# Optimization experiments

Hardware: AMD Instinct MI355X
Metric: run time of the kernel (lower is better)

## Reference

```python
import jax, jax.numpy as jnp
import numpy as np

B, N, K = 8, 2048, 16   # batch, points, neighbors (after dropping self)
EPS = 1e-5


def _bn(y, g, b, m, v):
    # eval-mode batchnorm over channel dim 1, y: [B,C,...]
    sh = (1, -1) + (1,) * (y.ndim - 2)
    inv = g.reshape(sh) / jnp.sqrt(v.reshape(sh) + EPS)
    return (y - m.reshape(sh)) * inv + b.reshape(sh)


def setup_inputs() -> dict:
    key = jax.random.key(0)
    ks = jax.random.split(key, 16)
    d = {}
    d["x"] = jax.random.normal(ks[0], (B, 3, N), dtype=jnp.float32)
    # pre: Conv1d(3->24, k=1) + BN
    d["w_pre"] = jax.random.normal(ks[1], (24, 3), dtype=jnp.float32) * 0.3
    d["b_pre"] = jax.random.normal(ks[2], (24,), dtype=jnp.float32) * 0.1
    d["g_pre"] = 1.0 + 0.1 * jax.random.normal(ks[3], (24,), dtype=jnp.float32)
    d["be_pre"] = 0.1 * jax.random.normal(ks[4], (24,), dtype=jnp.float32)
    d["m_pre"] = 0.1 * jax.random.normal(ks[5], (24,), dtype=jnp.float32)
    d["v_pre"] = jax.random.uniform(ks[6], (24,), minval=0.5, maxval=1.5, dtype=jnp.float32)
    # shared_mlp_1: Conv2d(48->12, 1, bias=False) + BN
    d["w1"] = jax.random.normal(ks[7], (12, 48), dtype=jnp.float32) * 0.15
    d["g1"] = 1.0 + 0.1 * jax.random.normal(ks[8], (12,), dtype=jnp.float32)
    d["be1"] = 0.1 * jax.random.normal(ks[9], (12,), dtype=jnp.float32)
    d["m1"] = 0.1 * jax.random.normal(ks[10], (12,), dtype=jnp.float32)
    d["v1"] = jax.random.uniform(ks[11], (12,), minval=0.5, maxval=1.5, dtype=jnp.float32)
    # shared_mlp_2: Conv2d(60->12, 1, bias=False) + BN
    d["w2"] = jax.random.normal(ks[12], (12, 60), dtype=jnp.float32) * 0.15
    d["g2"] = 1.0 + 0.1 * jax.random.normal(ks[13], (12,), dtype=jnp.float32)
    d["be2"] = 0.1 * jax.random.normal(ks[14], (12,), dtype=jnp.float32)
    d["m2"] = 0.1 * jax.random.normal(ks[15], (12,), dtype=jnp.float32)
    d["v2"] = jnp.ones((12,), dtype=jnp.float32)
    # shared_mlp_3: Conv2d(72->12, 1, bias=False), no BN
    d["w3"] = jax.random.normal(jax.random.fold_in(key, 99), (12, 72), dtype=jnp.float32) * 0.15
    return d


def reference(x, w_pre, b_pre, g_pre, be_pre, m_pre, v_pre,
              w1, g1, be1, m1, v1, w2, g2, be2, m2, v2, w3):
    # pre: 1x1 conv1d + BN + ReLU -> [B,24,N]
    pre = jnp.einsum('oc,bcn->bon', w_pre, x) + b_pre[None, :, None]
    pre = jax.nn.relu(_bn(pre, g_pre, be_pre, m_pre, v_pre))

    # kNN on xyz = x.detach(): [B,N,3]
    pts = jax.lax.stop_gradient(jnp.swapaxes(x, 1, 2))
    sq = jnp.sum(pts * pts, axis=-1)                              # [B,N]
    d2 = sq[:, :, None] + sq[:, None, :] - 2.0 * jnp.einsum('bnc,bmc->bnm', pts, pts)
    _, idx = jax.lax.top_k(-d2, K + 1)                             # nearest K+1 incl. self
    idx = idx[..., 1:]                                             # drop self -> [B,N,K]

    # gather neighbor features: [B,24,N,K]
    grouped = jax.vmap(lambda f, i: f[:, i])(pre, idx)
    center = jnp.broadcast_to(pre[..., None], grouped.shape)
    y = jnp.concatenate([center, grouped], axis=1)                 # [B,48,N,K]

    h1 = jax.nn.relu(_bn(jnp.einsum('oc,bcnk->bonk', w1, y), g1, be1, m1, v1))
    y = jnp.concatenate([h1, y], axis=1)                           # [B,60,N,K]
    h2 = jax.nn.relu(_bn(jnp.einsum('oc,bcnk->bonk', w2, y), g2, be2, m2, v2))
    y = jnp.concatenate([h2, y], axis=1)                           # [B,72,N,K]
    h3 = jnp.einsum('oc,bcnk->bonk', w3, y)
    y = jnp.concatenate([h3, y], axis=1)                           # [B,84,N,K]

    y = jnp.max(y, axis=-1)                                        # maxpool over neighbors -> [B,84,N]
    return jnp.concatenate([y, x], axis=1)                         # [B,87,N]
```

## Files before the change

kernel.cpp:

```cpp
#include <hip/hip_runtime.h>
#include <math.h>

#define EPS 1e-5f
#define NBATCH 8
#define NPTS 2048
#define KNB 16
#define BIG 3.2e38f

#define PRE_BLKS 32
#define KNN_BLKS (NBATCH * 64)
#define FUSED_LDS 54400

#define WS_PRE 0
#define WS_AUX (16384 * 24)
#define WS_IDX (WS_AUX + 16384 * 72)

__global__ __launch_bounds__(512) void fused_kernel(
    const float* __restrict__ x,
    const float* __restrict__ w_pre, const float* __restrict__ b_pre,
    const float* __restrict__ g_pre, const float* __restrict__ be_pre,
    const float* __restrict__ m_pre, const float* __restrict__ v_pre,
    const float* __restrict__ w1, const float* __restrict__ g1,
    const float* __restrict__ be1, const float* __restrict__ m1,
    const float* __restrict__ v1,
    const float* __restrict__ w2, const float* __restrict__ g2,
    const float* __restrict__ be2, const float* __restrict__ m2,
    const float* __restrict__ v2, const float* __restrict__ w3,
    float* __restrict__ pre, float* __restrict__ aux,
    int* __restrict__ knn_out) {
  extern __shared__ char smem[];
  int tid = threadIdx.x;
  if (blockIdx.x < PRE_BLKS) {
    float* fwp = (float*)smem;
    float* fbp = fwp + 72;
    float* fw1 = fbp + 24;
    float* fb1 = fw1 + 576;
    float* fw2 = fb1 + 12;
    float* fb2 = fw2 + 720;
    if (tid < 72) { int o = tid / 3; fwp[tid] = w_pre[tid] * (g_pre[o] / sqrtf(v_pre[o] + EPS)); }
    if (tid < 24) { float inv = g_pre[tid] / sqrtf(v_pre[tid] + EPS);
                    fbp[tid] = (b_pre[tid] - m_pre[tid]) * inv + be_pre[tid]; }
    for (int j = tid; j < 576; j += 512) { int o = j / 48; fw1[j] = w1[j] * (g1[o] / sqrtf(v1[o] + EPS)); }
    if (tid < 12) { float inv = g1[tid] / sqrtf(v1[tid] + EPS); fb1[tid] = be1[tid] - m1[tid] * inv; }
    for (int j = tid; j < 720; j += 512) { int o = j / 60; fw2[j] = w2[j] * (g2[o] / sqrtf(v2[o] + EPS)); }
    if (tid < 12) { float inv = g2[tid] / sqrtf(v2[tid] + EPS); fb2[tid] = be2[tid] - m2[tid] * inv; }
    __syncthreads();
    int p = blockIdx.x * 512 + tid;
    int b = p >> 11, n = p & (NPTS - 1);
    const float* xb = x + (size_t)b * 3 * NPTS;
    float x0 = xb[n], x1 = xb[NPTS + n], x2 = xb[2 * NPTS + n];
    float pr[24];
#pragma unroll
    for (int c = 0; c < 24; ++c) {
      float v = fmaf(fwp[c * 3 + 0], x0,
                fmaf(fwp[c * 3 + 1], x1,
                fmaf(fwp[c * 3 + 2], x2, fbp[c])));
      pr[c] = fmaxf(v, 0.f);
    }
    float4* o4 = (float4*)(pre + (size_t)p * 24);
#pragma unroll
    for (int i = 0; i < 6; ++i)
      o4[i] = make_float4(pr[4*i], pr[4*i+1], pr[4*i+2], pr[4*i+3]);
    float* A = aux + (size_t)p * 72;
#pragma unroll
    for (int o = 0; o < 12; ++o) {
      float u1 = fb1[o], a1 = 0.f, u2 = fb2[o], a2 = 0.f, u3 = 0.f, a3 = 0.f;
#pragma unroll
      for (int i = 0; i < 24; ++i) {
        u1 = fmaf(fw1[o*48 + i],      pr[i], u1);
        a1 = fmaf(fw1[o*48 + 24 + i], pr[i], a1);
        u2 = fmaf(fw2[o*60 + 12 + i], pr[i], u2);
        a2 = fmaf(fw2[o*60 + 36 + i], pr[i], a2);
        u3 = fmaf(w3[o*72 + 24 + i],  pr[i], u3);
        a3 = fmaf(w3[o*72 + 48 + i],  pr[i], a3);
      }
      A[o] = u1; A[12+o] = u2; A[24+o] = u3;
      A[36+o] = a1; A[48+o] = a2; A[60+o] = a3;
    }
    return;
  }
  float4* C4   = (float4*)smem;
  float* slist = (float*)(smem + 32768);
  float* sd2   = (float*)(smem + 49152);
  int*   sidx  = (int*)(smem + 51712);
  int*   scnt  = (int*)(smem + 54272);
  int bi = blockIdx.x - PRE_BLKS;
  int b = bi >> 6, chunk = bi & 63;
  const float* xb = x + (size_t)b * 3 * NPTS;
  for (int j = tid; j < NPTS; j += 512) {
    float xx = xb[j], yy = xb[NPTS + j], zz = xb[2 * NPTS + j];
    float sq = __fadd_rn(__fadd_rn(__fmul_rn(xx, xx), __fmul_rn(yy, yy)),
                         __fmul_rn(zz, zz));
    C4[j] = make_float4(2.0f * xx, 2.0f * yy, 2.0f * zz, sq);
  }
  for (int j = tid; j < 32 * 20; j += 512) sidx[j] = 0;
  if (tid < 32) scnt[tid] = 0;
  __syncthreads();
  int p = tid & 31, s = tid >> 5;
  int n = chunk * 32 + p;
  float4 me4 = C4[n];
  float mex = 0.5f * me4.x, mey = 0.5f * me4.y, mez = 0.5f * me4.z;
  float sqn = me4.w;
  const float4* Cs = C4 + s * 128;
  int selfc = n - s * 128;
  float L[16];
#pragma unroll
  for (int t = 0; t < 16; ++t) L[t] = BIG;
#pragma unroll 4
  for (int c = 0; c < 128; ++c) {
    float4 q = Cs[c];
    float dot2 = __fadd_rn(__fadd_rn(__fmul_rn(mex, q.x), __fmul_rn(mey, q.y)),
                           __fmul_rn(mez, q.z));
    float d2 = __fsub_rn(__fadd_rn(sqn, q.w), dot2);
    d2 = (c == selfc) ? BIG : d2;
#pragma unroll
    for (int t = 15; t >= 1; --t) L[t] = fminf(fmaxf(L[t-1], d2), L[t]);
    L[0] = fminf(L[0], d2);
  }
  {
    float bb[16], m16[16];
#pragma unroll
    for (int i = 0; i < 16; ++i) bb[i] = __shfl_xor(L[i], 32, 64);
#pragma unroll
    for (int i = 0; i < 16; ++i) m16[i] = fminf(L[i], bb[15 - i]);
#pragma unroll
    for (int d = 8; d >= 1; d >>= 1) {
#pragma unroll
      for (int i = 0; i < 16; ++i) {
        if (!(i & d)) {
          float lo = fminf(m16[i], m16[i | d]);
          float hi = fmaxf(m16[i], m16[i | d]);
          m16[i] = lo; m16[i | d] = hi;
        }
      }
    }
    if (!(s & 1)) {
#pragma unroll
      for (int i = 0; i < 16; ++i) slist[((s >> 1) * 16 + i) * 32 + p] = m16[i];
    }
  }
  __syncthreads();
  for (int W = 4; W >= 1; W >>= 1) {
    int w = tid >> 5;
    bool act = (w < W);
    float a[16], bb[16];
    if (act) {
#pragma unroll
      for (int i = 0; i < 16; ++i) a[i]  = slist[((2 * w) * 16 + i) * 32 + p];
#pragma unroll
      for (int i = 0; i < 16; ++i) bb[i] = slist[((2 * w + 1) * 16 + i) * 32 + p];
    }
    __syncthreads();
    if (act) {
      float m16[16];
#pragma unroll
      for (int i = 0; i < 16; ++i) m16[i] = fminf(a[i], bb[15 - i]);
#pragma unroll
      for (int d = 8; d >= 1; d >>= 1) {
#pragma unroll
        for (int i = 0; i < 16; ++i) {
          if (!(i & d)) {
            float lo = fminf(m16[i], m16[i | d]);
            float hi = fmaxf(m16[i], m16[i | d]);
            m16[i] = lo; m16[i | d] = hi;
          }
        }
      }
#pragma unroll
      for (int i = 0; i < 16; ++i) slist[(w * 16 + i) * 32 + p] = m16[i];
    }
    __syncthreads();
  }
  float tau = slist[15 * 32 + p];
#pragma unroll 4
  for (int c = 0; c < 128; ++c) {
    float4 q = Cs[c];
    float dot2 = __fadd_rn(__fadd_rn(__fmul_rn(mex, q.x), __fmul_rn(mey, q.y)),
                           __fmul_rn(mez, q.z));
    float d2 = __fsub_rn(__fadd_rn(sqn, q.w), dot2);
    int j = s * 128 + c;
    if (d2 <= tau && j != n) {
      int pos = atomicAdd(&scnt[p], 1);
      if (pos < 20) { sd2[p * 20 + pos] = d2; sidx[p * 20 + pos] = j; }
    }
  }
  __syncthreads();
  if (tid < 32) {
    int c = scnt[tid]; if (c > 20) c = 20;
    if (c > 16) {
      for (int t = 0; t < 16; ++t) {
        int best = t;
        for (int u = t + 1; u < c; ++u) {
          float da = sd2[tid * 20 + u], db = sd2[tid * 20 + best];
          int ia = sidx[tid * 20 + u], ib = sidx[tid * 20 + best];
          if (da < db || (da == db && ia < ib)) best = u;
        }
        float td = sd2[tid * 20 + t]; sd2[tid * 20 + t] = sd2[tid * 20 + best]; sd2[tid * 20 + best] = td;
        int ti = sidx[tid * 20 + t]; sidx[tid * 20 + t] = sidx[tid * 20 + best]; sidx[tid * 20 + best] = ti;
      }
    }
  }
  __syncthreads();
  {
    int pp = tid >> 4, kk = tid & 15;
    knn_out[((size_t)b * NPTS + chunk * 32 + pp) * KNB + kk] = sidx[pp * 20 + kk];
  }
}

__global__ __launch_bounds__(256) void mlp_kernel(
    const float* __restrict__ pre, const float* __restrict__ aux,
    const int* __restrict__ knn, const float* __restrict__ x,
    const float* __restrict__ w2, const float* __restrict__ g2,
    const float* __restrict__ v2, const float* __restrict__ w3,
    float* __restrict__ out) {
  __shared__ float sW2h[144], sW3h2[144], sW3h1[144];
  __shared__ float sout[87 * 16];
  int tid = threadIdx.x;
  if (tid < 144) {
    int o = tid / 12, i = tid - o * 12;
    float inv2 = g2[o] / sqrtf(v2[o] + EPS);
    sW2h[tid]  = w2[o * 60 + i] * inv2;
    sW3h2[tid] = w3[o * 72 + i];
    sW3h1[tid] = w3[o * 72 + 12 + i];
  }
  __syncthreads();
  int k = tid & 15, pl = tid >> 4;
  int p = blockIdx.x * 16 + pl;
  int b = p >> 11, n = p & (NPTS - 1);
  int nb = knn[(size_t)p * KNB + k];
  const float4* u4 = (const float4*)(aux + (size_t)p * 72);
  const float4* a4 = (const float4*)(aux + ((size_t)(b << 11) + nb) * 72 + 36);
  float uc[36], av[36];
#pragma unroll
  for (int i = 0; i < 9; ++i) {
    float4 t = u4[i];
    uc[4*i] = t.x; uc[4*i+1] = t.y; uc[4*i+2] = t.z; uc[4*i+3] = t.w;
    float4 t2 = a4[i];
    av[4*i] = t2.x; av[4*i+1] = t2.y; av[4*i+2] = t2.z; av[4*i+3] = t2.w;
  }
  float h1[12], h2[12], h3[12];
#pragma unroll
  for (int o = 0; o < 12; ++o) h1[o] = fmaxf(uc[o] + av[o], 0.f);
#pragma unroll
  for (int o = 0; o < 12; ++o) {
    float a = uc[12 + o] + av[12 + o];
#pragma unroll
    for (int i = 0; i < 12; ++i) a = fmaf(sW2h[o * 12 + i], h1[i], a);
    h2[o] = fmaxf(a, 0.f);
  }
#pragma unroll
  for (int o = 0; o < 12; ++o) {
    float a = uc[24 + o] + av[24 + o];
#pragma unroll
    for (int i = 0; i < 12; ++i) a = fmaf(sW3h2[o * 12 + i], h2[i], a);
#pragma unroll
    for (int i = 0; i < 12; ++i) a = fmaf(sW3h1[o * 12 + i], h1[i], a);
    h3[o] = a;
  }
  float nbf[24];
  const float4* pn4 = (const float4*)(pre + ((size_t)(b << 11) + nb) * 24);
#pragma unroll
  for (int i = 0; i < 6; ++i) {
    float4 t = pn4[i];
    nbf[4*i] = t.x; nbf[4*i+1] = t.y; nbf[4*i+2] = t.z; nbf[4*i+3] = t.w;
  }
#pragma unroll
  for (int m = 1; m < 16; m <<= 1) {
#pragma unroll
    for (int o = 0; o < 12; ++o) {
      h1[o] = fmaxf(h1[o], __shfl_xor(h1[o], m, 16));
      h2[o] = fmaxf(h2[o], __shfl_xor(h2[o], m, 16));
      h3[o] = fmaxf(h3[o], __shfl_xor(h3[o], m, 16));
    }
#pragma unroll
    for (int i = 0; i < 24; ++i)
      nbf[i] = fmaxf(nbf[i], __shfl_xor(nbf[i], m, 16));
  }
  if (k == 0) {
    const float4* c4 = (const float4*)(pre + (size_t)p * 24);
#pragma unroll
    for (int o = 0; o < 12; ++o) {
      sout[(0  + o) * 16 + pl] = h3[o];
      sout[(12 + o) * 16 + pl] = h2[o];
      sout[(24 + o) * 16 + pl] = h1[o];
    }
#pragma unroll
    for (int i = 0; i < 6; ++i) {
      float4 t = c4[i];
      sout[(36 + 4*i    ) * 16 + pl] = t.x;
      sout[(36 + 4*i + 1) * 16 + pl] = t.y;
      sout[(36 + 4*i + 2) * 16 + pl] = t.z;
      sout[(36 + 4*i + 3) * 16 + pl] = t.w;
    }
#pragma unroll
    for (int i = 0; i < 24; ++i) sout[(60 + i) * 16 + pl] = nbf[i];
    const float* xb = x + (size_t)b * 3 * NPTS + n;
    sout[84 * 16 + pl] = xb[0];
    sout[85 * 16 + pl] = xb[NPTS];
    sout[86 * 16 + pl] = xb[2 * NPTS];
  }
  __syncthreads();
  int n0 = (blockIdx.x * 16) & (NPTS - 1);
  float* ob = out + (size_t)b * 87 * NPTS;
  for (int j2 = tid; j2 < 87 * 16; j2 += 256) {
    int c = j2 >> 4, i = j2 & 15;
    ob[(size_t)c * NPTS + n0 + i] = sout[j2];
  }
}

extern "C" void kernel_launch(void* const* d_in, const int* in_sizes, int n_in,
                              void* d_out, int out_size, void* d_ws, size_t ws_size,
                              hipStream_t stream) {
  (void)in_sizes; (void)n_in; (void)out_size; (void)ws_size;
  const float* x     = (const float*)d_in[0];
  const float* w_pre = (const float*)d_in[1];
  const float* b_pre = (const float*)d_in[2];
  const float* g_pre = (const float*)d_in[3];
  const float* be_pre= (const float*)d_in[4];
  const float* m_pre = (const float*)d_in[5];
  const float* v_pre = (const float*)d_in[6];
  const float* w1    = (const float*)d_in[7];
  const float* g1    = (const float*)d_in[8];
  const float* be1   = (const float*)d_in[9];
  const float* m1    = (const float*)d_in[10];
  const float* v1    = (const float*)d_in[11];
  const float* w2    = (const float*)d_in[12];
  const float* g2    = (const float*)d_in[13];
  const float* be2   = (const float*)d_in[14];
  const float* m2    = (const float*)d_in[15];
  const float* v2    = (const float*)d_in[16];
  const float* w3    = (const float*)d_in[17];
  float* ws  = (float*)d_ws;
  float* pre = ws + WS_PRE;
  float* aux = ws + WS_AUX;
  int*   knn = (int*)(ws + WS_IDX);
  float* out = (float*)d_out;

  fused_kernel<<<PRE_BLKS + KNN_BLKS, 512, FUSED_LDS, stream>>>(
      x, w_pre, b_pre, g_pre, be_pre, m_pre, v_pre,
      w1, g1, be1, m1, v1, w2, g2, be2, m2, v2, w3,
      pre, aux, knn);
  mlp_kernel<<<NBATCH * NPTS / 16, 256, 0, stream>>>(pre, aux, knn, x,
                                                     w2, g2, v2, w3, out);
}
```

Before: 178.3 us.

## Fold pre-MLP into KNN blocks and batch top-K insertion with bitonic merges

Removes the separate pre-compute blocks: every KNN block now computes the pre features and aux partial products for its own 32 points, with 16 threads per point each handling one output channel. The per-candidate 16-deep insertion in the KNN scan is replaced by sorting chunks of 16 distances with a bitonic network and merging each chunk into the running list. The distance uses FMA instead of separately rounded multiplies and adds, and launch bounds request 4 blocks per CU. The FMA change can alter rounding, and with it the neighbor choice in near-tie cases, and the extra setup adds a sync to every KNN block.

```diff
diff --git a/kernel.cpp b/kernel.cpp
--- a/kernel.cpp
+++ b/kernel.cpp
@@ -7,7 +7,6 @@
 #define KNB 16
 #define BIG 3.2e38f
 
-#define PRE_BLKS 32
 #define KNN_BLKS (NBATCH * 64)
 #define FUSED_LDS 54400
 
@@ -15,7 +14,13 @@
 #define WS_AUX (16384 * 24)
 #define WS_IDX (WS_AUX + 16384 * 72)
 
-__global__ __launch_bounds__(512) void fused_kernel(
+__device__ __forceinline__ float dist2f(float mex, float mey, float mez,
+                                        float sqn, float4 q) {
+  float dot2 = fmaf(mex, q.x, fmaf(mey, q.y, __fmul_rn(mez, q.z)));
+  return __fsub_rn(__fadd_rn(sqn, q.w), dot2);
+}
+
+__global__ __launch_bounds__(512, 4) void fused_kernel(
     const float* __restrict__ x,
     const float* __restrict__ w_pre, const float* __restrict__ b_pre,
     const float* __restrict__ g_pre, const float* __restrict__ be_pre,
@@ -29,26 +34,45 @@
     float* __restrict__ pre, float* __restrict__ aux,
     int* __restrict__ knn_out) {
   extern __shared__ char smem[];
+  float4* C4   = (float4*)smem;
+  float* slist = (float*)(smem + 32768);
+  float* fwp = (float*)(smem + 32768);
+  float* fbp = fwp + 72;
+  float* fw1 = fbp + 24;
+  float* fb1 = fw1 + 576;
+  float* fw2 = fb1 + 12;
+  float* fb2 = fw2 + 720;
+  float* sd2   = (float*)(smem + 49152);
+  int*   sidx  = (int*)(smem + 51712);
+  int*   scnt  = (int*)(smem + 54272);
+
   int tid = threadIdx.x;
-  if (blockIdx.x < PRE_BLKS) {
-    float* fwp = (float*)smem;
-    float* fbp = fwp + 72;
-    float* fw1 = fbp + 24;
-    float* fb1 = fw1 + 576;
-    float* fw2 = fb1 + 12;
-    float* fb2 = fw2 + 720;
-    if (tid < 72) { int o = tid / 3; fwp[tid] = w_pre[tid] * (g_pre[o] / sqrtf(v_pre[o] + EPS)); }
-    if (tid < 24) { float inv = g_pre[tid] / sqrtf(v_pre[tid] + EPS);
-                    fbp[tid] = (b_pre[tid] - m_pre[tid]) * inv + be_pre[tid]; }
-    for (int j = tid; j < 576; j += 512) { int o = j / 48; fw1[j] = w1[j] * (g1[o] / sqrtf(v1[o] + EPS)); }
-    if (tid < 12) { float inv = g1[tid] / sqrtf(v1[tid] + EPS); fb1[tid] = be1[tid] - m1[tid] * inv; }
-    for (int j = tid; j < 720; j += 512) { int o = j / 60; fw2[j] = w2[j] * (g2[o] / sqrtf(v2[o] + EPS)); }
-    if (tid < 12) { float inv = g2[tid] / sqrtf(v2[tid] + EPS); fb2[tid] = be2[tid] - m2[tid] * inv; }
-    __syncthreads();
-    int p = blockIdx.x * 512 + tid;
-    int b = p >> 11, n = p & (NPTS - 1);
-    const float* xb = x + (size_t)b * 3 * NPTS;
-    float x0 = xb[n], x1 = xb[NPTS + n], x2 = xb[2 * NPTS + n];
+  int bi = blockIdx.x;
+  int b = bi >> 6, chunk = bi & 63;
+  const float* xb = x + (size_t)b * 3 * NPTS;
+
+  for (int j = tid; j < NPTS; j += 512) {
+    float xx = xb[j], yy = xb[NPTS + j], zz = xb[2 * NPTS + j];
+    float sq = __fadd_rn(__fadd_rn(__fmul_rn(xx, xx), __fmul_rn(yy, yy)),
+                         __fmul_rn(zz, zz));
+    C4[j] = make_float4(2.0f * xx, 2.0f * yy, 2.0f * zz, sq);
+  }
+  if (tid < 72) { int o = tid / 3; fwp[tid] = w_pre[tid] * (g_pre[o] / sqrtf(v_pre[o] + EPS)); }
+  if (tid < 24) { float inv = g_pre[tid] / sqrtf(v_pre[tid] + EPS);
+                  fbp[tid] = (b_pre[tid] - m_pre[tid]) * inv + be_pre[tid]; }
+  for (int j = tid; j < 576; j += 512) { int o = j / 48; fw1[j] = w1[j] * (g1[o] / sqrtf(v1[o] + EPS)); }
+  if (tid < 12) { float inv = g1[tid] / sqrtf(v1[tid] + EPS); fb1[tid] = be1[tid] - m1[tid] * inv; }
+  for (int j = tid; j < 720; j += 512) { int o = j / 60; fw2[j] = w2[j] * (g2[o] / sqrtf(v2[o] + EPS)); }
+  if (tid < 12) { float inv = g2[tid] / sqrtf(v2[tid] + EPS); fb2[tid] = be2[tid] - m2[tid] * inv; }
+  for (int j = tid; j < 32 * 20; j += 512) sidx[j] = 0;
+  if (tid < 32) scnt[tid] = 0;
+  __syncthreads();
+
+  {
+    int r = tid & 15, pt = tid >> 4;
+    int n0 = chunk * 32 + pt;
+    size_t pgl = (size_t)(b << 11) + n0;
+    float x0 = xb[n0], x1 = xb[NPTS + n0], x2 = xb[2 * NPTS + n0];
     float pr[24];
 #pragma unroll
     for (int c = 0; c < 24; ++c) {
@@ -57,13 +81,14 @@
                 fmaf(fwp[c * 3 + 2], x2, fbp[c])));
       pr[c] = fmaxf(v, 0.f);
     }
-    float4* o4 = (float4*)(pre + (size_t)p * 24);
-#pragma unroll
-    for (int i = 0; i < 6; ++i)
-      o4[i] = make_float4(pr[4*i], pr[4*i+1], pr[4*i+2], pr[4*i+3]);
-    float* A = aux + (size_t)p * 72;
-#pragma unroll
-    for (int o = 0; o < 12; ++o) {
+    if (r == 0) {
+      float4* o4 = (float4*)(pre + pgl * 24);
+#pragma unroll
+      for (int i = 0; i < 6; ++i)
+        o4[i] = make_float4(pr[4*i], pr[4*i+1], pr[4*i+2], pr[4*i+3]);
+    }
+    if (r < 12) {
+      int o = r;
       float u1 = fb1[o], a1 = 0.f, u2 = fb2[o], a2 = 0.f, u3 = 0.f, a3 = 0.f;
 #pragma unroll
       for (int i = 0; i < 24; ++i) {
@@ -74,28 +99,13 @@
         u3 = fmaf(w3[o*72 + 24 + i],  pr[i], u3);
         a3 = fmaf(w3[o*72 + 48 + i],  pr[i], a3);
       }
-      A[o] = u1; A[12+o] = u2; A[24+o] = u3;
-      A[36+o] = a1; A[48+o] = a2; A[60+o] = a3;
-    }
-    return;
-  }
-  float4* C4   = (float4*)smem;
-  float* slist = (float*)(smem + 32768);
-  float* sd2   = (float*)(smem + 49152);
-  int*   sidx  = (int*)(smem + 51712);
-  int*   scnt  = (int*)(smem + 54272);
-  int bi = blockIdx.x - PRE_BLKS;
-  int b = bi >> 6, chunk = bi & 63;
-  const float* xb = x + (size_t)b * 3 * NPTS;
-  for (int j = tid; j < NPTS; j += 512) {
-    float xx = xb[j], yy = xb[NPTS + j], zz = xb[2 * NPTS + j];
-    float sq = __fadd_rn(__fadd_rn(__fmul_rn(xx, xx), __fmul_rn(yy, yy)),
-                         __fmul_rn(zz, zz));
-    C4[j] = make_float4(2.0f * xx, 2.0f * yy, 2.0f * zz, sq);
-  }
-  for (int j = tid; j < 32 * 20; j += 512) sidx[j] = 0;
-  if (tid < 32) scnt[tid] = 0;
-  __syncthreads();
+      float* A = aux + pgl * 72;
+      A[o] = u1; A[12 + o] = u2; A[24 + o] = u3;
+      A[36 + o] = a1; A[48 + o] = a2; A[60 + o] = a3;
+    }
+  }
+  __syncthreads();
+
   int p = tid & 31, s = tid >> 5;
   int n = chunk * 32 + p;
   float4 me4 = C4[n];
@@ -106,16 +116,48 @@
   float L[16];
 #pragma unroll
   for (int t = 0; t < 16; ++t) L[t] = BIG;
-#pragma unroll 4
-  for (int c = 0; c < 128; ++c) {
-    float4 q = Cs[c];
-    float dot2 = __fadd_rn(__fadd_rn(__fmul_rn(mex, q.x), __fmul_rn(mey, q.y)),
-                           __fmul_rn(mez, q.z));
-    float d2 = __fsub_rn(__fadd_rn(sqn, q.w), dot2);
-    d2 = (c == selfc) ? BIG : d2;
-#pragma unroll
-    for (int t = 15; t >= 1; --t) L[t] = fminf(fmaxf(L[t-1], d2), L[t]);
-    L[0] = fminf(L[0], d2);
+  for (int c0 = 0; c0 < 128; c0 += 16) {
+    float S[16];
+#pragma unroll
+    for (int cc = 0; cc < 16; ++cc) {
+      float4 q = Cs[c0 + cc];
+      float d2 = dist2f(mex, mey, mez, sqn, q);
+      S[cc] = ((c0 + cc) == selfc) ? BIG : d2;
+    }
+#pragma unroll
+    for (int pw = 1; pw < 16; pw <<= 1) {
+#pragma unroll
+      for (int k = pw; k >= 1; k >>= 1) {
+#pragma unroll
+        for (int j = (k & (pw - 1)); j + k < 16; j += 2 * k) {
+#pragma unroll
+          for (int i = 0; i < k; ++i) {
+            int a = i + j, bq = i + j + k;
+            if (bq < 16 && (a / (2 * pw) == bq / (2 * pw))) {
+              float lo = fminf(S[a], S[bq]);
+              float hi = fmaxf(S[a], S[bq]);
+              S[a] = lo; S[bq] = hi;
+            }
+          }
+        }
+      }
+    }
+    float m[16];
+#pragma unroll
+    for (int i = 0; i < 16; ++i) m[i] = fminf(L[i], S[15 - i]);
+#pragma unroll
+    for (int d = 8; d >= 1; d >>= 1) {
+#pragma unroll
+      for (int i = 0; i < 16; ++i) {
+        if (!(i & d)) {
+          float lo = fminf(m[i], m[i | d]);
+          float hi = fmaxf(m[i], m[i | d]);
+          m[i] = lo; m[i | d] = hi;
+        }
+      }
+    }
+#pragma unroll
+    for (int i = 0; i < 16; ++i) L[i] = m[i];
   }
   {
     float bb[16], m16[16];
@@ -175,9 +217,7 @@
 #pragma unroll 4
   for (int c = 0; c < 128; ++c) {
     float4 q = Cs[c];
-    float dot2 = __fadd_rn(__fadd_rn(__fmul_rn(mex, q.x), __fmul_rn(mey, q.y)),
-                           __fmul_rn(mez, q.z));
-    float d2 = __fsub_rn(__fadd_rn(sqn, q.w), dot2);
+    float d2 = dist2f(mex, mey, mez, sqn, q);
     int j = s * 128 + c;
     if (d2 <= tau && j != n) {
       int pos = atomicAdd(&scnt[p], 1);
@@ -336,7 +376,7 @@
   int*   knn = (int*)(ws + WS_IDX);
   float* out = (float*)d_out;
 
-  fused_kernel<<<PRE_BLKS + KNN_BLKS, 512, FUSED_LDS, stream>>>(
+  fused_kernel<<<KNN_BLKS, 512, FUSED_LDS, stream>>>(
       x, w_pre, b_pre, g_pre, be_pre, m_pre, v_pre,
       w1, g1, be1, m1, v1, w2, g2, be2, m2, v2, w3,
       pre, aux, knn);
```

Result: faster. 156.0 us (-12.5%).
